# Performance work log

Hardware: AMD Instinct MI355X
Metric: run time of the kernel (lower is better)

Reference implementation:

```python
import jax, jax.numpy as jnp
import numpy as np

B, C_IN, C_OUT, A, H, W = 32, 256, 512, 256, 64, 64


def setup_inputs() -> dict:
    key = jax.random.key(0)
    ks = jax.random.split(key, 8)
    s = 0.02
    return {
        "x": jax.random.normal(ks[0], (B, C_IN, H, W), dtype=jnp.float32),
        "g": jax.random.normal(ks[1], (B, C_OUT), dtype=jnp.float32),
        "Wg": jax.random.normal(ks[2], (A, C_OUT), dtype=jnp.float32) * s,
        "bg": jnp.full((A,), 0.1, dtype=jnp.float32),
        "Wx": jax.random.normal(ks[3], (A, C_IN), dtype=jnp.float32) * s,
        "bx": jnp.full((A,), 0.1, dtype=jnp.float32),
        "Wf": jax.random.normal(ks[4], (1, A), dtype=jnp.float32) * s,
        "bf": jnp.full((1,), 0.1, dtype=jnp.float32),
    }


def reference(x, g, Wg, bg, Wx, bx, Wf, bf):
    b, c, h, w = x.shape
    gg = g @ Wg.T + bg                                  # [B, A]
    xf = x.reshape(b, c, h * w)                          # [B, C, HW]
    # Linear_x applied per spatial position (batched instead of python loop)
    nx = jnp.einsum('bcn,ac->bna', xf, Wx) + bx          # [B, HW, A]
    nx = jax.nn.relu(gg[:, None, :] + nx)                # [B, HW, A]
    att = jnp.einsum('bna,a->bn', nx, Wf[0]) + bf[0]     # [B, HW]
    # min-subtract, sum-divide normalization
    att = att - jnp.min(att, axis=1, keepdims=True)
    att = att / jnp.sum(att, axis=1, keepdims=True)
    out = jnp.einsum('bcn,bn->bc', xf, att)              # weighted pooling [B, C]
    return out, att.reshape(b, h, w)
```

## Files before the change

### kernel.cpp

```cpp
#include <hip/hip_runtime.h>
#include <stdint.h>

#define B_   32
#define CIN  256
#define COUT 512
#define A_   256
#define HW_  4096
#define NT   64
#define TILES 8

typedef short  short8  __attribute__((ext_vector_type(8)));
typedef float  float4_ __attribute__((ext_vector_type(4)));

__device__ __forceinline__ unsigned f2bf(float f) {
    unsigned u = __float_as_uint(f);
    u += 0x7FFFu + ((u >> 16) & 1u);
    return u >> 16;
}
__device__ __forceinline__ float bf2f(unsigned h) {
    return __uint_as_float(h << 16);
}

__global__ __launch_bounds__(256) void prep_kernel(
    const float* __restrict__ g, const float* __restrict__ Wg,
    const float* __restrict__ bg, const float* __restrict__ Wx,
    const float* __restrict__ bx,
    uint4* __restrict__ WxR, float* __restrict__ ggbx,
    float* __restrict__ P, float* __restrict__ T)
{
    int t = threadIdx.x;
    if (blockIdx.x >= 32) {
        int e = (blockIdx.x - 32) * 256 + t;
        int lane = e & 63, ai = (e >> 6) & 3, kk = (e >> 8) & 7, w = e >> 11;
        int a  = w * 64 + ai * 16 + (lane & 15);
        int kb = kk * 32 + (lane >> 4) * 8;
        const float4* s = (const float4*)(Wx + (size_t)a * 256 + kb);
        float4 u0 = s[0], u1 = s[1];
        uint4 pk;
        pk.x = f2bf(u0.x) | (f2bf(u0.y) << 16);
        pk.y = f2bf(u0.z) | (f2bf(u0.w) << 16);
        pk.z = f2bf(u1.x) | (f2bf(u1.y) << 16);
        pk.w = f2bf(u1.z) | (f2bf(u1.w) << 16);
        WxR[e] = pk;
        return;
    }
    int b = blockIdx.x;
    int i = b * 256 + t;
    P[i] = 0.f; T[i] = 0.f;

    __shared__ float gl[COUT];
    gl[t]       = g[b * COUT + t];
    gl[t + 256] = g[b * COUT + 256 + t];
    __syncthreads();

    float acc0 = bg[t] + bx[t], acc1 = 0.f;
    const float4* wr = (const float4*)(Wg + (size_t)t * COUT);
    #pragma unroll 8
    for (int co = 0; co < COUT / 4; co += 2) {
        float4 wv0 = wr[co],     gv0 = *(const float4*)&gl[co * 4];
        float4 wv1 = wr[co + 1], gv1 = *(const float4*)&gl[co * 4 + 4];
        acc0 += wv0.x * gv0.x + wv0.y * gv0.y + wv0.z * gv0.z + wv0.w * gv0.w;
        acc1 += wv1.x * gv1.x + wv1.y * gv1.y + wv1.z * gv1.z + wv1.w * gv1.w;
    }
    ggbx[b * 256 + t] = acc0 + acc1;
}

__global__ __launch_bounds__(512)
__attribute__((amdgpu_waves_per_eu(2, 2)))
void attn_main(
    const float* __restrict__ x, const char* __restrict__ WxR,
    const float* __restrict__ ggbx, const float* __restrict__ Wf,
    const float* __restrict__ bfs,
    float* __restrict__ P, float* __restrict__ T, float* __restrict__ raw)
{
    __shared__ unsigned int xT[2][NT * 128];
    __shared__ float att_part[8][NT];
    __shared__ float raw_l[NT];

    int bid = blockIdx.x;
    int b = bid >> 3, tg = bid & 7;
    int t = threadIdx.x, w = t >> 6, lane = t & 63;
    int quad = lane >> 4, l15 = lane & 15;
    int st = (tg + b) & 7;

    const float* xb = x + (size_t)b * CIN * HW_ + tg * (TILES * NT);

    short8 bfp[16];
    {
        const char* wsl = WxR + (w >> 1) * 32768 + (w & 1) * 2048 + lane * 16;
        #pragma unroll
        for (int kk = 0; kk < 8; kk++) {
            bfp[kk * 2]     = *(const short8*)(wsl + kk * 4096);
            bfp[kk * 2 + 1] = *(const short8*)(wsl + kk * 4096 + 1024);
        }
    }

    float4_ ga4[2], wf4[2];
    #pragma unroll
    for (int ai = 0; ai < 2; ai++) {
        int a0 = w * 32 + ai * 16 + quad * 4;
        ga4[ai] = *(const float4_*)&ggbx[b * 256 + a0];
        wf4[ai] = *(const float4_*)&Wf[a0];
    }

    int n4 = l15 * 4;
    int cb = w * 32 + quad * 8;
    int qc = cb >> 3;
    const float* xrow = xb + (size_t)cb * HW_ + n4;

    float4_ v[8];
    #pragma unroll
    for (int j = 0; j < 8; j++)
        v[j] = *(const float4_*)(xrow + st * NT + (size_t)j * HW_);
    #pragma unroll
    for (int r = 0; r < 4; r++) {
        uint4 pk;
        pk.x = f2bf(v[0][r]) | (f2bf(v[1][r]) << 16);
        pk.y = f2bf(v[2][r]) | (f2bf(v[3][r]) << 16);
        pk.z = f2bf(v[4][r]) | (f2bf(v[5][r]) << 16);
        pk.w = f2bf(v[6][r]) | (f2bf(v[7][r]) << 16);
        int n = n4 + r;
        *(uint4*)&xT[0][n * 128 + ((qc ^ (n & 31)) << 2)] = pk;
    }

    float pp[4] = {0.f, 0.f, 0.f, 0.f};
    float tt[4] = {0.f, 0.f, 0.f, 0.f};
    int qpt   = (t & 63) >> 1;
    int half  = (t & 1) * 8;
    int nbase = w * 8;

    __syncthreads();

    #pragma unroll 1
    for (int ii = 0; ii < TILES; ii++) {
        int it = (ii + st) & 7;
        const unsigned int* xl = xT[ii & 1];
        unsigned int* xw = xT[(ii + 1) & 1];

        if (ii < TILES - 1) {
            int itn = (ii + 1 + st) & 7;
            const float* xn = xrow + itn * NT;
            #pragma unroll
            for (int j = 0; j < 8; j++)
                v[j] = *(const float4_*)(xn + (size_t)j * HW_);
        }
        __builtin_amdgcn_sched_barrier(0);

        float4_ acc[4][2];
        #pragma unroll
        for (int mi = 0; mi < 4; mi++) {
            acc[mi][0] = (float4_){0.f, 0.f, 0.f, 0.f};
            acc[mi][1] = (float4_){0.f, 0.f, 0.f, 0.f};
        }
        short8 afA[4], afB[4];
        auto LDA = [&](short8* af, int k0) {
            int qk = (k0 >> 3) + quad;
            #pragma unroll
            for (int mi = 0; mi < 4; mi++) {
                int n = mi * 16 + l15;
                af[mi] = *(const short8*)&xl[n * 128 + ((qk ^ (n & 31)) << 2)];
            }
        };
        auto MM = [&](short8* af, int ks) {
            #pragma unroll
            for (int mi = 0; mi < 4; mi++) {
                acc[mi][0] = __builtin_amdgcn_mfma_f32_16x16x32_bf16(
                    bfp[ks * 2],     af[mi], acc[mi][0], 0, 0, 0);
                acc[mi][1] = __builtin_amdgcn_mfma_f32_16x16x32_bf16(
                    bfp[ks * 2 + 1], af[mi], acc[mi][1], 0, 0, 0);
            }
        };

        LDA(afA, 0);   LDA(afB, 32);
        MM(afA, 0);    LDA(afA, 64);
        MM(afB, 1);    LDA(afB, 96);
        MM(afA, 2);    LDA(afA, 128);
        MM(afB, 3);    LDA(afB, 160);
        MM(afA, 4);    LDA(afA, 192);
        MM(afB, 5);    LDA(afB, 224);
        MM(afA, 6);
        MM(afB, 7);

        #pragma unroll
        for (int mi = 0; mi < 4; mi++) {
            float p = 0.f;
            #pragma unroll
            for (int ai = 0; ai < 2; ai++) {
                #pragma unroll
                for (int r = 0; r < 4; r++) {
                    float vv = fmaxf(acc[mi][ai][r] + ga4[ai][r], 0.f);
                    p = fmaf(vv, wf4[ai][r], p);
                }
            }
            p += __shfl_xor(p, 16, 64);
            p += __shfl_xor(p, 32, 64);
            if (quad == 0) att_part[w][mi * 16 + l15] = p;
        }
        __syncthreads();

        if (t < NT) {
            float rv = att_part[0][t] + att_part[1][t] + att_part[2][t] + att_part[3][t]
                     + att_part[4][t] + att_part[5][t] + att_part[6][t] + att_part[7][t]
                     + bfs[0];
            raw[b * HW_ + (tg * TILES + it) * NT + t] = rv;
            raw_l[t] = rv;
        }
        __syncthreads();

        #pragma unroll
        for (int i = 0; i < 8; i++) {
            int n = nbase + i;
            uint2 u = *(const uint2*)((const char*)xl + n * 512 + ((qpt ^ (n & 31)) << 4) + half);
            float rv = raw_l[n];
            float x0 = bf2f(u.x & 0xFFFFu), x1 = bf2f(u.x >> 16);
            float x2 = bf2f(u.y & 0xFFFFu), x3 = bf2f(u.y >> 16);
            pp[0] = fmaf(x0, rv, pp[0]); tt[0] += x0;
            pp[1] = fmaf(x1, rv, pp[1]); tt[1] += x1;
            pp[2] = fmaf(x2, rv, pp[2]); tt[2] += x2;
            pp[3] = fmaf(x3, rv, pp[3]); tt[3] += x3;
        }

        if (ii < TILES - 1) {
            #pragma unroll
            for (int r = 0; r < 4; r++) {
                uint4 pk;
                pk.x = f2bf(v[0][r]) | (f2bf(v[1][r]) << 16);
                pk.y = f2bf(v[2][r]) | (f2bf(v[3][r]) << 16);
                pk.z = f2bf(v[4][r]) | (f2bf(v[5][r]) << 16);
                pk.w = f2bf(v[6][r]) | (f2bf(v[7][r]) << 16);
                int n = n4 + r;
                *(uint4*)&xw[n * 128 + ((qc ^ (n & 31)) << 2)] = pk;
            }
        }
        __syncthreads();
    }

    {
        float* red = (float*)xT;
        float4_* pr = (float4_*)(red + w * 512);
        float4_* tr = (float4_*)(red + w * 512 + 256);
        pr[lane] = (float4_){pp[0], pp[1], pp[2], pp[3]};
        tr[lane] = (float4_){tt[0], tt[1], tt[2], tt[3]};
        __syncthreads();
        int sel = t >> 8, cc = t & 255;
        float s = 0.f;
        #pragma unroll
        for (int g = 0; g < 8; g++)
            s += red[g * 512 + sel * 256 + cc];
        atomicAdd((sel ? T : P) + b * 256 + cc, s);
    }
}

__global__ __launch_bounds__(256) void finalize_kernel(
    const float* __restrict__ raw, const float* __restrict__ P,
    const float* __restrict__ T, float* __restrict__ out)
{
    int b = blockIdx.x, t = threadIdx.x;
    const float* r = raw + (size_t)b * HW_;
    float v[16];
    float mn = 3.4e38f, sm = 0.f;
    #pragma unroll
    for (int i = 0; i < 16; i++) {
        v[i] = r[t + 256 * i];
        mn = fminf(mn, v[i]);
        sm += v[i];
    }
    #pragma unroll
    for (int off = 1; off < 64; off <<= 1) {
        mn = fminf(mn, __shfl_xor(mn, off, 64));
        sm += __shfl_xor(sm, off, 64);
    }
    __shared__ float smn[4], ssm[4];
    int w = t >> 6;
    if ((t & 63) == 0) { smn[w] = mn; ssm[w] = sm; }
    __syncthreads();
    mn = fminf(fminf(smn[0], smn[1]), fminf(smn[2], smn[3]));
    sm = (ssm[0] + ssm[1]) + (ssm[2] + ssm[3]);
    float S = sm - 4096.f * mn;
    float inv = 1.f / S;

    float* att = out + B_ * CIN + (size_t)b * HW_;
    #pragma unroll
    for (int i = 0; i < 16; i++) att[t + 256 * i] = (v[i] - mn) * inv;

    int ic = b * 256 + t;
    out[ic] = (P[ic] - mn * T[ic]) * inv;
}

extern "C" void kernel_launch(void* const* d_in, const int* in_sizes, int n_in,
                              void* d_out, int out_size, void* d_ws, size_t ws_size,
                              hipStream_t stream)
{
    const float* x   = (const float*)d_in[0];
    const float* g   = (const float*)d_in[1];
    const float* Wg  = (const float*)d_in[2];
    const float* bg  = (const float*)d_in[3];
    const float* Wx  = (const float*)d_in[4];
    const float* bx  = (const float*)d_in[5];
    const float* Wf  = (const float*)d_in[6];
    const float* bf  = (const float*)d_in[7];
    float* out = (float*)d_out;

    char* wsb = (char*)d_ws;
    uint4* WxR  = (uint4*)wsb;
    float* ggbx = (float*)(wsb + 131072);
    float* P    = ggbx + 8192;
    float* T    = P + 8192;
    float* raw  = T + 8192;

    prep_kernel<<<64, 256, 0, stream>>>(g, Wg, bg, Wx, bx, WxR, ggbx, P, T);
    attn_main<<<256, 512, 0, stream>>>(x, (const char*)WxR, ggbx, Wf, bf, P, T, raw);
    finalize_kernel<<<32, 256, 0, stream>>>(raw, P, T, out);
}
```

Measured before the change: 232.2 us.

## Stage x tiles asynchronously into LDS with global_load_lds and relax barriers

Replaces the register-held prefetch of the next x tile with direct global-to-LDS async loads into a new fp32 staging buffer. Each tile is then converted to transposed bf16 from LDS at the start of the iteration. Two inner barriers now wait only on LDS counters, so the async global loads can stay in flight across them. This frees registers and removes the global-load latency from the compute path, at the cost of 64KB of extra LDS, an extra LDS round trip for conversion and a different barrier structure.

```diff
diff --git a/kernel.cpp b/kernel.cpp
--- a/kernel.cpp
+++ b/kernel.cpp
@@ -12,6 +12,9 @@
 typedef short  short8  __attribute__((ext_vector_type(8)));
 typedef float  float4_ __attribute__((ext_vector_type(4)));
 
+typedef const __attribute__((address_space(1))) unsigned int glb_uint;
+typedef __attribute__((address_space(3))) unsigned int lds_uint;
+
 __device__ __forceinline__ unsigned f2bf(float f) {
     unsigned u = __float_as_uint(f);
     u += 0x7FFFu + ((u >> 16) & 1u);
@@ -19,6 +22,13 @@
 }
 __device__ __forceinline__ float bf2f(unsigned h) {
     return __uint_as_float(h << 16);
+}
+
+__device__ __forceinline__ void bar_lds() {
+    __builtin_amdgcn_sched_barrier(0);
+    asm volatile("s_waitcnt lgkmcnt(0)" ::: "memory");
+    __builtin_amdgcn_s_barrier();
+    __builtin_amdgcn_sched_barrier(0);
 }
 
 __global__ __launch_bounds__(256) void prep_kernel(
@@ -73,6 +83,7 @@
     const float* __restrict__ bfs,
     float* __restrict__ P, float* __restrict__ T, float* __restrict__ raw)
 {
+    __shared__ float        rawb[CIN * NT];
     __shared__ unsigned int xT[2][NT * 128];
     __shared__ float att_part[8][NT];
     __shared__ float raw_l[NT];
@@ -84,6 +95,17 @@
     int st = (tg + b) & 7;
 
     const float* xb = x + (size_t)b * CIN * HW_ + tg * (TILES * NT);
+
+    auto STAGE = [&](int tile) {
+        const float* gb = xb + (size_t)(w * 32 + (lane >> 4)) * HW_
+                             + tile * NT + (lane & 15) * 4;
+        #pragma unroll
+        for (int j = 0; j < 8; j++) {
+            __builtin_amdgcn_global_load_lds(
+                (glb_uint*)(gb + (size_t)j * 4 * HW_),
+                (lds_uint*)&rawb[(w * 8 + j) * 256], 16, 0, 0);
+        }
+    };
 
     short8 bfp[16];
     {
@@ -103,49 +125,41 @@
         wf4[ai] = *(const float4_*)&Wf[a0];
     }
 
-    int n4 = l15 * 4;
-    int cb = w * 32 + quad * 8;
-    int qc = cb >> 3;
-    const float* xrow = xb + (size_t)cb * HW_ + n4;
-
-    float4_ v[8];
-    #pragma unroll
-    for (int j = 0; j < 8; j++)
-        v[j] = *(const float4_*)(xrow + st * NT + (size_t)j * HW_);
-    #pragma unroll
-    for (int r = 0; r < 4; r++) {
-        uint4 pk;
-        pk.x = f2bf(v[0][r]) | (f2bf(v[1][r]) << 16);
-        pk.y = f2bf(v[2][r]) | (f2bf(v[3][r]) << 16);
-        pk.z = f2bf(v[4][r]) | (f2bf(v[5][r]) << 16);
-        pk.w = f2bf(v[6][r]) | (f2bf(v[7][r]) << 16);
-        int n = n4 + r;
-        *(uint4*)&xT[0][n * 128 + ((qc ^ (n & 31)) << 2)] = pk;
-    }
-
     float pp[4] = {0.f, 0.f, 0.f, 0.f};
     float tt[4] = {0.f, 0.f, 0.f, 0.f};
     int qpt   = (t & 63) >> 1;
     int half  = (t & 1) * 8;
     int nbase = w * 8;
 
-    __syncthreads();
+    STAGE(st);
 
     #pragma unroll 1
     for (int ii = 0; ii < TILES; ii++) {
         int it = (ii + st) & 7;
-        const unsigned int* xl = xT[ii & 1];
-        unsigned int* xw = xT[(ii + 1) & 1];
-
-        if (ii < TILES - 1) {
-            int itn = (ii + 1 + st) & 7;
-            const float* xn = xrow + itn * NT;
+        unsigned int* xc = xT[ii & 1];
+
+        __syncthreads();
+
+        {
+            int n = lane;
             #pragma unroll
-            for (int j = 0; j < 8; j++)
-                v[j] = *(const float4_*)(xn + (size_t)j * HW_);
-        }
-        __builtin_amdgcn_sched_barrier(0);
-
+            for (int p = 0; p < 4; p++) {
+                int q = w * 4 + p;
+                const float* rb = &rawb[(q * 8) * 64 + n];
+                uint4 pk;
+                pk.x = f2bf(rb[0])   | (f2bf(rb[64])  << 16);
+                pk.y = f2bf(rb[128]) | (f2bf(rb[192]) << 16);
+                pk.z = f2bf(rb[256]) | (f2bf(rb[320]) << 16);
+                pk.w = f2bf(rb[384]) | (f2bf(rb[448]) << 16);
+                *(uint4*)&xc[n * 128 + ((q ^ (n & 31)) << 2)] = pk;
+            }
+        }
+        __syncthreads();
+
+        if (ii < TILES - 1)
+            STAGE((ii + 1 + st) & 7);
+
+        const unsigned int* xl = xc;
         float4_ acc[4][2];
         #pragma unroll
         for (int mi = 0; mi < 4; mi++) {
@@ -196,7 +210,7 @@
             p += __shfl_xor(p, 32, 64);
             if (quad == 0) att_part[w][mi * 16 + l15] = p;
         }
-        __syncthreads();
+        bar_lds();
 
         if (t < NT) {
             float rv = att_part[0][t] + att_part[1][t] + att_part[2][t] + att_part[3][t]
@@ -205,7 +219,7 @@
             raw[b * HW_ + (tg * TILES + it) * NT + t] = rv;
             raw_l[t] = rv;
         }
-        __syncthreads();
+        bar_lds();
 
         #pragma unroll
         for (int i = 0; i < 8; i++) {
@@ -219,20 +233,6 @@
             pp[2] = fmaf(x2, rv, pp[2]); tt[2] += x2;
             pp[3] = fmaf(x3, rv, pp[3]); tt[3] += x3;
         }
-
-        if (ii < TILES - 1) {
-            #pragma unroll
-            for (int r = 0; r < 4; r++) {
-                uint4 pk;
-                pk.x = f2bf(v[0][r]) | (f2bf(v[1][r]) << 16);
-                pk.y = f2bf(v[2][r]) | (f2bf(v[3][r]) << 16);
-                pk.z = f2bf(v[4][r]) | (f2bf(v[5][r]) << 16);
-                pk.w = f2bf(v[6][r]) | (f2bf(v[7][r]) << 16);
-                int n = n4 + r;
-                *(uint4*)&xw[n * 128 + ((qc ^ (n & 31)) << 2)] = pk;
-            }
-        }
-        __syncthreads();
     }
 
     {
```

Result: no change. 232.1 us (-0.0%).
